# Kernel optimization log

Hardware: AMD Instinct MI355X
Metric: run time of the kernel (lower is better)

The kernel has to match this reference:

```python
import jax, jax.numpy as jnp
import numpy as np

N_NODES = 100000
N_EDGES = 1600000
NFEAT = 256
NHID = 128
NCLASS = 2
NEG_SLOPE = 0.2


def setup_inputs() -> dict:
    key = jax.random.key(0)
    ks = jax.random.split(key, 8)
    x = jax.random.normal(ks[0], (N_NODES, NFEAT), dtype=jnp.float32)
    edge_index = jax.random.randint(ks[1], (2, N_EDGES), 0, N_NODES, dtype=jnp.int64)
    # GATConv params (heads=1): lin weight (no bias), att_src, att_dst, bias
    W = jax.random.normal(ks[2], (NFEAT, NHID), dtype=jnp.float32) * (1.0 / np.sqrt(NFEAT))
    att_src = jax.random.normal(ks[3], (NHID,), dtype=jnp.float32) * (1.0 / np.sqrt(NHID))
    att_dst = jax.random.normal(ks[4], (NHID,), dtype=jnp.float32) * (1.0 / np.sqrt(NHID))
    bias_gat = jnp.zeros((NHID,), dtype=jnp.float32)
    fc_w = jax.random.normal(ks[5], (NCLASS, NHID), dtype=jnp.float32) * (1.0 / np.sqrt(NHID))
    fc_b = jnp.zeros((NCLASS,), dtype=jnp.float32)
    return {"x": x, "edge_index": edge_index, "W": W, "att_src": att_src,
            "att_dst": att_dst, "bias_gat": bias_gat, "fc_w": fc_w, "fc_b": fc_b}


def reference(x, edge_index, W, att_src, att_dst, bias_gat, fc_w, fc_b):
    N = x.shape[0]
    # add self loops (PyG GATConv default)
    loops = jnp.broadcast_to(jnp.arange(N, dtype=edge_index.dtype)[None, :], (2, N))
    ei = jnp.concatenate([edge_index, loops], axis=1)  # [2, E+N]
    src, dst = ei[0], ei[1]

    h = x @ W                                 # [N, NHID]
    a_src = h @ att_src                       # [N]
    a_dst = h @ att_dst                       # [N]

    e = jax.nn.leaky_relu(a_src[src] + a_dst[dst], NEG_SLOPE)  # [E+N]
    # segment softmax over destination nodes (every node has a self loop)
    m = jax.ops.segment_max(e, dst, num_segments=N)
    ex = jnp.exp(e - m[dst])
    s = jax.ops.segment_sum(ex, dst, num_segments=N)
    alpha = ex / (s[dst] + 1e-16)             # [E+N]

    msg = h[src] * alpha[:, None]             # [E+N, NHID]
    out = jax.ops.segment_sum(msg, dst, num_segments=N) + bias_gat  # [N, NHID]

    logits = out @ fc_w.T + fc_b              # [N, NCLASS]
    return jax.nn.log_softmax(logits, axis=1)
```

## Files before the change

### kernel.cpp

```cpp
#include <hip/hip_runtime.h>
#include <hip/hip_bf16.h>
#include <stdint.h>

#define N_NODES 100000
#define N_EDGES 1600000
#define NFEAT   256
#define NHID    128
#define NEG_SLOPE 0.2f

#define NB_B       1563
#define SLAB       2048
#define BIN_BLOCKS 128

typedef __attribute__((ext_vector_type(8))) short short8;
typedef __attribute__((ext_vector_type(4))) float f32x4;

__device__ __forceinline__ int clamp_node(int v) {
    unsigned u = (unsigned)v;
    return (u < (unsigned)N_NODES) ? (int)u : 0;
}

__device__ __forceinline__ unsigned short f2bf(float f) {
    unsigned u = __float_as_uint(f);
    return (unsigned short)((u + 0x7fffu + ((u >> 16) & 1u)) >> 16);
}
__device__ __forceinline__ unsigned pkbf(float a, float b) {
    __hip_bfloat162 t = __float22bfloat162_rn(make_float2(a, b));
    return *reinterpret_cast<unsigned*>(&t);
}
__device__ __forceinline__ float bflo(unsigned p) { return __uint_as_float(p << 16); }
__device__ __forceinline__ float bfhi(unsigned p) { return __uint_as_float(p & 0xffff0000u); }

__global__ __launch_bounds__(256) void k_conv(
    const float* __restrict__ W, unsigned short* __restrict__ Wt)
{
    int id = blockIdx.x * 256 + threadIdx.x;
    int n = id >> 8, k = id & 255;
    Wt[id] = f2bf(W[k * NHID + n]);
}

#define LDS_STRIDE 40
__global__ __launch_bounds__(256) void k_gemm_mfma(
    const float* __restrict__ x,
    const unsigned short* __restrict__ Wt,
    const float* __restrict__ atts,
    const float* __restrict__ attd,
    unsigned short* __restrict__ hb,
    float* __restrict__ asrc,
    float* __restrict__ adst)
{
    __shared__ unsigned short As[128 * LDS_STRIDE];
    __shared__ unsigned short Bs[128 * LDS_STRIDE];
    __shared__ float satt[128][2];

    const int tid  = threadIdx.x;
    const int wave = tid >> 6;
    const int lane = tid & 63;
    const int wm = wave >> 1, wn = wave & 1;
    const int lr = lane & 15, q = lane >> 4;
    const int blockM = blockIdx.x * 128;

    const int sr = tid >> 1;
    const int hh = tid & 1;

    if (tid < 128) { satt[tid][0] = 0.f; satt[tid][1] = 0.f; }

    f32x4 acc[4][4];
#pragma unroll
    for (int a = 0; a < 4; ++a)
#pragma unroll
        for (int b = 0; b < 4; ++b) acc[a][b] = 0.f;

    const int growA = min(blockM + sr, N_NODES - 1);
    const float* xrow = x + (size_t)growA * NFEAT + hh * 16;
    const unsigned short* wrow = Wt + sr * NFEAT + hh * 16;

    for (int kt = 0; kt < 8; ++kt) {
        const float4* xp = (const float4*)(xrow + kt * 32);
        float4 v0 = xp[0], v1 = xp[1], v2 = xp[2], v3 = xp[3];
        uint4 pa0 = make_uint4(pkbf(v0.x, v0.y), pkbf(v0.z, v0.w),
                               pkbf(v1.x, v1.y), pkbf(v1.z, v1.w));
        uint4 pa1 = make_uint4(pkbf(v2.x, v2.y), pkbf(v2.z, v2.w),
                               pkbf(v3.x, v3.y), pkbf(v3.z, v3.w));
        uint4 pb0 = *(const uint4*)(wrow + kt * 32);
        uint4 pb1 = *(const uint4*)(wrow + kt * 32 + 8);

        __syncthreads();
        *(uint4*)&As[sr * LDS_STRIDE + hh * 16 + 0] = pa0;
        *(uint4*)&As[sr * LDS_STRIDE + hh * 16 + 8] = pa1;
        *(uint4*)&Bs[sr * LDS_STRIDE + hh * 16 + 0] = pb0;
        *(uint4*)&Bs[sr * LDS_STRIDE + hh * 16 + 8] = pb1;
        __syncthreads();

        short8 af[4], bfr[4];
#pragma unroll
        for (int mt = 0; mt < 4; ++mt)
            af[mt] = *(const short8*)&As[(wm * 64 + mt * 16 + lr) * LDS_STRIDE + q * 8];
#pragma unroll
        for (int nt = 0; nt < 4; ++nt)
            bfr[nt] = *(const short8*)&Bs[(wn * 64 + nt * 16 + lr) * LDS_STRIDE + q * 8];

#pragma unroll
        for (int mt = 0; mt < 4; ++mt)
#pragma unroll
            for (int nt = 0; nt < 4; ++nt)
                acc[mt][nt] = __builtin_amdgcn_mfma_f32_16x16x32_bf16(
                    af[mt], bfr[nt], acc[mt][nt], 0, 0, 0);
    }

    float attsv[4], attdv[4];
#pragma unroll
    for (int nt = 0; nt < 4; ++nt) {
        attsv[nt] = atts[wn * 64 + nt * 16 + lr];
        attdv[nt] = attd[wn * 64 + nt * 16 + lr];
    }
#pragma unroll
    for (int mt = 0; mt < 4; ++mt) {
#pragma unroll
        for (int reg = 0; reg < 4; ++reg) {
            float s = 0.f, d = 0.f;
#pragma unroll
            for (int nt = 0; nt < 4; ++nt) {
                float v = acc[mt][nt][reg];
                s += v * attsv[nt];
                d += v * attdv[nt];
            }
#pragma unroll
            for (int mask = 8; mask > 0; mask >>= 1) {
                s += __shfl_xor(s, mask);
                d += __shfl_xor(d, mask);
            }
            if (lr == 0) {
                int lrow = wm * 64 + mt * 16 + q * 4 + reg;
                atomicAdd(&satt[lrow][0], s);
                atomicAdd(&satt[lrow][1], d);
            }
        }
    }

#pragma unroll
    for (int mt = 0; mt < 4; ++mt) {
#pragma unroll
        for (int reg = 0; reg < 4; ++reg) {
            int grow = blockM + wm * 64 + mt * 16 + q * 4 + reg;
            if (grow < N_NODES) {
                unsigned short* hp = hb + (size_t)grow * NHID + wn * 64 + lr;
#pragma unroll
                for (int nt = 0; nt < 4; ++nt)
                    hp[nt * 16] = f2bf(acc[mt][nt][reg]);
            }
        }
    }

    __syncthreads();
    if (tid < 128) {
        int g = blockM + tid;
        if (g < N_NODES) {
            asrc[g] = satt[tid][0];
            adst[g] = satt[tid][1];
        }
    }
}

__global__ __launch_bounds__(256) void k_bin(
    const int* __restrict__ ei, int* __restrict__ gcur,
    unsigned* __restrict__ staged)
{
    __shared__ int hist[NB_B];
    __shared__ int base[NB_B];
    const int t = threadIdx.x;
    const int per = (N_EDGES + BIN_BLOCKS - 1) / BIN_BLOCKS;
    const int e0 = blockIdx.x * per;
    const int e1 = min(e0 + per, N_EDGES);

    for (int i = t; i < NB_B; i += 256) hist[i] = 0;
    __syncthreads();
    for (int e = e0 + t; e < e1; e += 256)
        atomicAdd(&hist[clamp_node(ei[N_EDGES + e]) >> 6], 1);
    __syncthreads();
    for (int i = t; i < NB_B; i += 256) {
        int c = hist[i];
        base[i] = c ? atomicAdd(&gcur[i], c) : 0;
        hist[i] = 0;
    }
    __syncthreads();
    for (int e = e0 + t; e < e1; e += 256) {
        int d = clamp_node(ei[N_EDGES + e]);
        int s = clamp_node(ei[e]);
        int b = d >> 6;
        int pos = base[b] + atomicAdd(&hist[b], 1);
        if (pos < SLAB)
            staged[(size_t)b * SLAB + pos] = (unsigned)s | ((unsigned)(d & 63) << 17);
    }
}

__global__ __launch_bounds__(256) void k_bsort(
    const unsigned* __restrict__ staged, const int* __restrict__ gcur,
    const float* __restrict__ asrc, const float* __restrict__ adst,
    float2* __restrict__ meta, int* __restrict__ noff, int* __restrict__ ncnt)
{
    __shared__ float2 buf[SLAB];
    __shared__ int hist[64], scanv[64];
    __shared__ float adst_s[64];

    const int b = blockIdx.x;
    const int t = threadIdx.x;
    const int eb = b * SLAB;
    const int n = min(gcur[b], SLAB);
    const int nodeStart = b * 64;

    if (t < 64) {
        hist[t] = 0;
        int gi = nodeStart + t;
        adst_s[t] = (gi < N_NODES) ? adst[gi] : 0.f;
    }
    __syncthreads();

    for (int j = t; j < n; j += 256)
        atomicAdd(&hist[(staged[eb + j] >> 17) & 63], 1);
    __syncthreads();

    if (t == 0) {
        int acc = 0;
        for (int i = 0; i < 64; ++i) { scanv[i] = acc; acc += hist[i]; }
    }
    __syncthreads();

    if (t < 64) {
        int gi = nodeStart + t;
        if (gi < N_NODES) { noff[gi] = eb + scanv[t]; ncnt[gi] = hist[t]; }
        hist[t] = 0;
    }
    __syncthreads();

    for (int j = t; j < n; j += 256) {
        unsigned pk = staged[eb + j];
        int s  = pk & 0x1FFFF;
        int dl = (pk >> 17) & 63;
        float a = asrc[s] + adst_s[dl];
        a = (a > 0.f) ? a : NEG_SLOPE * a;
        float ew = __expf(fminf(a, 60.f));
        int pos = scanv[dl] + atomicAdd(&hist[dl], 1);
        buf[pos] = make_float2(__int_as_float(s), ew);
    }
    __syncthreads();
    for (int j = t; j < n; j += 256) meta[eb + j] = buf[j];
}

__global__ __launch_bounds__(256) void k_agg(
    const unsigned short* __restrict__ hb, const float* __restrict__ asrc,
    const float* __restrict__ adst, const int* __restrict__ noff,
    const int* __restrict__ ncnt, const float2* __restrict__ meta,
    const float* __restrict__ bias, const float* __restrict__ fcw,
    const float* __restrict__ fcb, float* __restrict__ out)
{
    const int wave = threadIdx.x >> 6;
    const int lane = threadIdx.x & 63;
    const int i = blockIdx.x * 4 + wave;
    if (i >= N_NODES) return;

    const unsigned* hrows = (const unsigned*)hb;

    float e0 = asrc[i] + adst[i];
    e0 = (e0 > 0.f) ? e0 : NEG_SLOPE * e0;
    float w = __expf(fminf(e0, 60.f));
    unsigned pself = hrows[(size_t)i * 64 + lane];
    float accx = w * bflo(pself), accy = w * bfhi(pself), ssum = w;

    const int jb = noff[i];
    const int n  = ncnt[i];
    const float2* mp = meta + jb;
    int j = 0;
    for (; j + 8 <= n; j += 8) {
        float2 m[8];
        unsigned p[8];
#pragma unroll
        for (int u = 0; u < 8; ++u) m[u] = mp[j + u];
#pragma unroll
        for (int u = 0; u < 8; ++u)
            p[u] = hrows[(size_t)__float_as_int(m[u].x) * 64 + lane];
#pragma unroll
        for (int u = 0; u < 8; ++u) {
            accx += m[u].y * bflo(p[u]);
            accy += m[u].y * bfhi(p[u]);
            ssum += m[u].y;
        }
    }
    for (; j < n; ++j) {
        float2 m = mp[j];
        unsigned p = hrows[(size_t)__float_as_int(m.x) * 64 + lane];
        accx += m.y * bflo(p);
        accy += m.y * bfhi(p);
        ssum += m.y;
    }

    float inv = 1.0f / (ssum + 1e-16f);
    float ox = accx * inv + bias[2 * lane];
    float oy = accy * inv + bias[2 * lane + 1];

    float l0 = ox * fcw[2 * lane] + oy * fcw[2 * lane + 1];
    float l1 = ox * fcw[NHID + 2 * lane] + oy * fcw[NHID + 2 * lane + 1];
#pragma unroll
    for (int off = 32; off > 0; off >>= 1) {
        l0 += __shfl_down(l0, off);
        l1 += __shfl_down(l1, off);
    }
    if (lane == 0) {
        l0 += fcb[0];
        l1 += fcb[1];
        float m = fmaxf(l0, l1);
        float ls = m + __logf(__expf(l0 - m) + __expf(l1 - m));
        ((float2*)out)[i] = make_float2(l0 - ls, l1 - ls);
    }
}

extern "C" void kernel_launch(void* const* d_in, const int* in_sizes, int n_in,
                              void* d_out, int out_size, void* d_ws, size_t ws_size,
                              hipStream_t stream)
{
    const float* x    = (const float*)d_in[0];
    const int*   ei   = (const int*)d_in[1];
    const float* W    = (const float*)d_in[2];
    const float* atts = (const float*)d_in[3];
    const float* attd = (const float*)d_in[4];
    const float* bias = (const float*)d_in[5];
    const float* fcw  = (const float*)d_in[6];
    const float* fcb  = (const float*)d_in[7];
    float*       out  = (float*)d_out;

    char* base = (char*)d_ws;
    size_t off = 0;
    auto carve = [&](size_t bytes) -> char* {
        char* p = base + off;
        off = (off + bytes + 255) & ~(size_t)255;
        return p;
    };
    unsigned short* hb     = (unsigned short*)carve((size_t)N_NODES * NHID * 2);
    float*          asrc   = (float*)carve(N_NODES * 4);
    float*          adst   = (float*)carve(N_NODES * 4);
    int*            gcur   = (int*)carve(NB_B * 4);
    int*            noff   = (int*)carve(N_NODES * 4);
    int*            ncnt   = (int*)carve(N_NODES * 4);
    unsigned*       staged = (unsigned*)carve((size_t)NB_B * SLAB * 4);
    float2*         meta   = (float2*)carve((size_t)NB_B * SLAB * 8);
    unsigned short* Wt     = (unsigned short*)carve(NHID * NFEAT * 2);
    (void)ws_size; (void)in_sizes; (void)n_in; (void)out_size;

    hipMemsetAsync(gcur, 0, NB_B * 4, stream);

    const int GB = (N_NODES + 127) / 128;

    k_conv<<<(NHID * NFEAT) / 256, 256, 0, stream>>>(W, Wt);
    k_gemm_mfma<<<GB, 256, 0, stream>>>(x, Wt, atts, attd, hb, asrc, adst);
    k_bin<<<BIN_BLOCKS, 256, 0, stream>>>(ei, gcur, staged);
    k_bsort<<<NB_B, 256, 0, stream>>>(staged, gcur, asrc, adst, meta, noff, ncnt);
    k_agg<<<(N_NODES + 3) / 4, 256, 0, stream>>>(hb, asrc, adst, noff, ncnt, meta,
                                                 bias, fcw, fcb, out);
}
```

Before: 355.5 us.

## Prefetch GEMM tiles, parallelize bucket scan, and raise binning block count

The GEMM main loop now loads the next K-tile of x and W into registers while MFMAs run on the current tile, so global-load latency overlaps compute. The per-bucket serial 64-element prefix scan done by one thread becomes a wavefront shuffle scan across 64 lanes. The binning kernel's block count rises from 128 to 512 to expose more parallelism. Together these target load latency, a serial bottleneck and occupancy, at the cost of more live registers in the GEMM.

```diff
diff --git a/kernel.cpp b/kernel.cpp
--- a/kernel.cpp
+++ b/kernel.cpp
@@ -10,7 +10,7 @@
 
 #define NB_B       1563
 #define SLAB       2048
-#define BIN_BLOCKS 128
+#define BIN_BLOCKS 512
 
 typedef __attribute__((ext_vector_type(8))) short short8;
 typedef __attribute__((ext_vector_type(4))) float f32x4;
@@ -75,22 +75,33 @@
     const float* xrow = x + (size_t)growA * NFEAT + hh * 16;
     const unsigned short* wrow = Wt + sr * NFEAT + hh * 16;
 
+    float4 va0, va1, va2, va3;
+    uint4  vb0, vb1;
+    {
+        const float4* xp = (const float4*)xrow;
+        va0 = xp[0]; va1 = xp[1]; va2 = xp[2]; va3 = xp[3];
+        vb0 = *(const uint4*)(wrow);
+        vb1 = *(const uint4*)(wrow + 8);
+    }
+
     for (int kt = 0; kt < 8; ++kt) {
-        const float4* xp = (const float4*)(xrow + kt * 32);
-        float4 v0 = xp[0], v1 = xp[1], v2 = xp[2], v3 = xp[3];
-        uint4 pa0 = make_uint4(pkbf(v0.x, v0.y), pkbf(v0.z, v0.w),
-                               pkbf(v1.x, v1.y), pkbf(v1.z, v1.w));
-        uint4 pa1 = make_uint4(pkbf(v2.x, v2.y), pkbf(v2.z, v2.w),
-                               pkbf(v3.x, v3.y), pkbf(v3.z, v3.w));
-        uint4 pb0 = *(const uint4*)(wrow + kt * 32);
-        uint4 pb1 = *(const uint4*)(wrow + kt * 32 + 8);
-
         __syncthreads();
+        uint4 pa0 = make_uint4(pkbf(va0.x, va0.y), pkbf(va0.z, va0.w),
+                               pkbf(va1.x, va1.y), pkbf(va1.z, va1.w));
+        uint4 pa1 = make_uint4(pkbf(va2.x, va2.y), pkbf(va2.z, va2.w),
+                               pkbf(va3.x, va3.y), pkbf(va3.z, va3.w));
         *(uint4*)&As[sr * LDS_STRIDE + hh * 16 + 0] = pa0;
         *(uint4*)&As[sr * LDS_STRIDE + hh * 16 + 8] = pa1;
-        *(uint4*)&Bs[sr * LDS_STRIDE + hh * 16 + 0] = pb0;
-        *(uint4*)&Bs[sr * LDS_STRIDE + hh * 16 + 8] = pb1;
+        *(uint4*)&Bs[sr * LDS_STRIDE + hh * 16 + 0] = vb0;
+        *(uint4*)&Bs[sr * LDS_STRIDE + hh * 16 + 8] = vb1;
         __syncthreads();
+
+        if (kt < 7) {
+            const float4* xp = (const float4*)(xrow + (kt + 1) * 32);
+            va0 = xp[0]; va1 = xp[1]; va2 = xp[2]; va3 = xp[3];
+            vb0 = *(const uint4*)(wrow + (kt + 1) * 32);
+            vb1 = *(const uint4*)(wrow + (kt + 1) * 32 + 8);
+        }
 
         short8 af[4], bfr[4];
 #pragma unroll
@@ -220,9 +231,15 @@
         atomicAdd(&hist[(staged[eb + j] >> 17) & 63], 1);
     __syncthreads();
 
-    if (t == 0) {
-        int acc = 0;
-        for (int i = 0; i < 64; ++i) { scanv[i] = acc; acc += hist[i]; }
+    if (t < 64) {
+        int v = hist[t];
+        int sc = v;
+#pragma unroll
+        for (int off = 1; off < 64; off <<= 1) {
+            int u = __shfl_up(sc, off);
+            if (t >= off) sc += u;
+        }
+        scanv[t] = sc - v;
     }
     __syncthreads();
 
```

After: 335.3 us. -5.7%, faster.
